# Kernel tuning notes

Measured on AMD Instinct MI355X. Metric: run time of the kernel, lower is better.

## Reference

```python
import jax, jax.numpy as jnp
import numpy as np

N, D_MODEL, D_PE, H = 4096, 512, 16, 8


def setup_inputs() -> dict:
    key = jax.random.key(0)
    ks = jax.random.split(key, 6)
    s = 1.0 / np.sqrt(D_MODEL)
    return {
        "x": jax.random.normal(ks[0], (N, D_MODEL), dtype=jnp.float32),
        "pe": jax.random.normal(ks[1], (N, D_PE), dtype=jnp.float32),
        "w_qkv": jax.random.normal(ks[2], (D_MODEL, 3 * D_MODEL), dtype=jnp.float32) * s,
        "b_qkv": jnp.zeros((3 * D_MODEL,), dtype=jnp.float32),
        "w_pe": jax.random.normal(ks[3], (D_PE, H), dtype=jnp.float32) * (1.0 / np.sqrt(D_PE)),
        "b_pe": jnp.zeros((H,), dtype=jnp.float32),
        "w_out": jax.random.normal(ks[4], (D_MODEL, D_MODEL), dtype=jnp.float32) * s,
        "b_out": jnp.zeros((D_MODEL,), dtype=jnp.float32),
    }


def reference(x, pe, w_qkv, b_qkv, w_pe, b_pe, w_out, b_out):
    n, d = x.shape
    h = w_pe.shape[1]
    hd = d // h
    scale = hd ** -0.5

    qkv = (x @ w_qkv + b_qkv).reshape(n, 3, h, hd)  # [N,3,H,hd]
    q = jnp.transpose(qkv[:, 0], (1, 0, 2))  # [H,N,hd]
    k = jnp.transpose(qkv[:, 1], (1, 0, 2))
    v = jnp.transpose(qkv[:, 2], (1, 0, 2))

    pe_proj = pe @ w_pe + b_pe  # [N,H]
    # bias[h,i,j] = pe_proj[j,h] - pe_proj[i,h]  (matches torch unsqueeze/permute)
    pt = pe_proj.T  # [H,N]
    bias = pt[:, None, :] - pt[:, :, None]  # [H,N,N]

    scores = jnp.einsum('hnd,hmd->hnm', q, k) * scale + bias  # [H,N,N]
    attn = jax.nn.softmax(scores, axis=-1)
    out = jnp.einsum('hnm,hmd->hnd', attn, v)  # [H,N,hd]
    out = jnp.transpose(out, (1, 0, 2)).reshape(n, d)
    return out @ w_out + b_out
```

## Files before the change

kernel.cpp:

```cpp
#include <hip/hip_runtime.h>
#include <stdint.h>
#include <stddef.h>


typedef unsigned short u16;
typedef __attribute__((ext_vector_type(8))) short short8;
typedef __attribute__((ext_vector_type(8))) unsigned short us8;
typedef __attribute__((ext_vector_type(4))) unsigned short us4;
typedef __attribute__((ext_vector_type(4))) float floatx4;

__device__ __forceinline__ u16 f2b(float f) {
  union { float f; uint32_t u; } v; v.f = f;
  uint32_t u = v.u;
  return (u16)((u + 0x7fffu + ((u >> 16) & 1u)) >> 16);
}

__device__ __forceinline__ uint32_t pkbf16(float a, float b) {
  union { float f; uint32_t u; } x, y; x.f = a; y.f = b;
  return __builtin_amdgcn_perm(y.u + 0x8000u, x.u + 0x8000u, 0x07060302u);
}

#if __has_builtin(__builtin_amdgcn_exp2f)
__device__ __forceinline__ float fexp2(float x) { return __builtin_amdgcn_exp2f(x); }
#else
__device__ __forceinline__ float fexp2(float x) { return exp2f(x); }
#endif

__device__ __forceinline__ void gld16(const u16* g, u16* l) {
  __builtin_amdgcn_global_load_lds(
      (const __attribute__((address_space(1))) uint32_t*)(const void*)g,
      (__attribute__((address_space(3))) uint32_t*)(void*)l, 16, 0, 0);
}


__device__ __forceinline__ void tr_tile(const float* __restrict__ in,
                                        u16* __restrict__ out, int R, int C,
                                        int bx, int by, u16 (*tile)[33]) {
  int tx = threadIdx.x & 31, ty = threadIdx.x >> 5;
  int c0 = bx * 32, r0 = by * 32;
#pragma unroll
  for (int i = 0; i < 32; i += 8)
    tile[ty + i][tx] = f2b(in[(size_t)(r0 + ty + i) * C + c0 + tx]);
  __syncthreads();
#pragma unroll
  for (int i = 0; i < 32; i += 8)
    out[(size_t)(c0 + ty + i) * R + r0 + tx] = tile[tx][ty + i];
}

__global__ __launch_bounds__(256) void k_prep(
    const float* __restrict__ x, u16* __restrict__ xb,
    const float* __restrict__ w_qkv, u16* __restrict__ wqkvT,
    const float* __restrict__ w_out, u16* __restrict__ woutT,
    const float* __restrict__ pe, const float* __restrict__ w_pe,
    const float* __restrict__ b_pe, float* __restrict__ wexp,
    u16* __restrict__ wpb) {
  __shared__ u16 tile[32][33];
  int b = blockIdx.x;
  if (b < 2048) {
    int i = b * 256 + threadIdx.x;
    float4 v = ((const float4*)x)[i];
    uint2 o = make_uint2(pkbf16(v.x, v.y), pkbf16(v.z, v.w));
    ((uint2*)xb)[i] = o;
  } else if (b < 2816) {
    int idx = b - 2048;
    tr_tile(w_qkv, wqkvT, 512, 1536, idx % 48, idx / 48, tile);
  } else if (b < 3072) {
    int idx = b - 2816;
    tr_tile(w_out, woutT, 512, 512, idx % 16, idx / 16, tile);
  } else {
    int idx = (b - 3072) * 256 + threadIdx.x;
    int h = idx >> 12, n = idx & 4095;
    float acc = b_pe[h];
#pragma unroll
    for (int d = 0; d < 16; ++d) acc = fmaf(pe[n * 16 + d], w_pe[d * 8 + h], acc);
    float w = exp2f(acc * 1.4426950408889634f - 16.0f);
    u16 wb = f2b(w);
    union { uint32_t u; float f; } cv; cv.u = ((uint32_t)wb) << 16;
    wexp[h * 4096 + n] = cv.f;
    int pn = (n & ~31) | (((n >> 2) & 3) << 3) | (((n >> 4) & 1) << 2) | (n & 3);
    wpb[h * 4096 + pn] = wb;
  }
}


__global__ __launch_bounds__(512, 6) void k_gemm_qkv(const u16* __restrict__ A,
                                                     const u16* __restrict__ Bt,
                                                     const float* __restrict__ bias,
                                                     const float* __restrict__ wexp,
                                                     u16* __restrict__ qk,
                                                     u16* __restrict__ vtp) {
  __shared__ __align__(16) u16 smem[24576];
  const int tid = threadIdx.x;
  const int lane = tid & 63, wave = tid >> 6;
  const int colx = lane & 15, quad = lane >> 4;
  const int m0 = blockIdx.y * 64, n0 = blockIdx.x * 128;
  const int wm = wave >> 2, wn = wave & 3;
  const int sc = (lane & 7) ^ ((lane >> 3) & 7);
  const floatx4 fz = {0.f, 0.f, 0.f, 0.f};
  floatx4 acc[2][2];
#pragma unroll
  for (int i = 0; i < 2; ++i)
#pragma unroll
    for (int j = 0; j < 2; ++j) acc[i][j] = fz;

#define PREF_QKV(k0, b)                                                       \
  {                                                                           \
    int rowa = wave * 8 + (lane >> 3);                                        \
    gld16(&A[(size_t)(m0 + rowa) * 512 + (k0) + sc * 8],                      \
          &smem[(b) * 4096 + wave * 512 + lane * 8]);                         \
    _Pragma("unroll") for (int c = 0; c < 2; ++c) {                           \
      int rowb = wave * 16 + c * 8 + (lane >> 3);                             \
      gld16(&Bt[(size_t)(n0 + rowb) * 512 + (k0) + sc * 8],                   \
            &smem[8192 + (b) * 8192 + wave * 1024 + c * 512 + lane * 8]);     \
    }                                                                         \
  }

  PREF_QKV(0, 0);
  __syncthreads();
  for (int it = 0; it < 8; ++it) {
    int cur = it & 1;
    if (it < 7) PREF_QKV((it + 1) * 64, cur ^ 1);
    const u16* As = &smem[cur * 4096];
    const u16* Bs = &smem[8192 + cur * 8192];
#pragma unroll
    for (int kk = 0; kk < 2; ++kk) {
      short8 af[2], bf[2];
#pragma unroll
      for (int i = 0; i < 2; ++i) {
        int row = wm * 32 + i * 16 + colx;
        af[i] = *(const short8*)&As[row * 64 + (((kk * 4 + quad) ^ (colx & 7))) * 8];
      }
#pragma unroll
      for (int j = 0; j < 2; ++j) {
        int row = wn * 32 + j * 16 + colx;
        bf[j] = *(const short8*)&Bs[row * 64 + (((kk * 4 + quad) ^ (colx & 7))) * 8];
      }
#pragma unroll
      for (int i = 0; i < 2; ++i)
#pragma unroll
        for (int j = 0; j < 2; ++j)
          acc[i][j] = __builtin_amdgcn_mfma_f32_16x16x32_bf16(af[i], bf[j], acc[i][j], 0, 0, 0);
    }
    __syncthreads();
  }

  const bool isV = (blockIdx.x >= 8);
  if (!isV) {
#pragma unroll
    for (int j = 0; j < 2; ++j) {
      int c = n0 + wn * 32 + j * 16 + colx;
      float bq = bias[c];
      float qs = (c < 512) ? 0.18033688011112042f : 1.0f;
#pragma unroll
      for (int i = 0; i < 2; ++i)
#pragma unroll
        for (int r = 0; r < 4; ++r) {
          int row = m0 + wm * 32 + i * 16 + quad * 4 + r;
          qk[(size_t)row * 1024 + c] = f2b((acc[i][j][r] + bq) * qs);
        }
    }
  } else {
    const int dv = n0 - 1024;
    u16* Vl = smem;
    const int hh = (dv + wn * 32) >> 6;
#pragma unroll
    for (int j = 0; j < 2; ++j) {
      float bq = bias[n0 + wn * 32 + j * 16 + colx];
#pragma unroll
      for (int i = 0; i < 2; ++i) {
        floatx4 wv = *(const floatx4*)&wexp[hh * 4096 + m0 + wm * 32 + i * 16 + quad * 4];
        us4 o;
#pragma unroll
        for (int r = 0; r < 4; ++r) o[r] = f2b((acc[i][j][r] + bq) * wv[r]);
        int dl = wn * 32 + j * 16 + colx;
        int nc = wm * 32 + quad * 8 + i * 4;
        *(us4*)&Vl[dl * 72 + nc] = o;
      }
    }
    __syncthreads();
#pragma unroll
    for (int t = 0; t < 2; ++t) {
      int idx = t * 512 + tid;
      int dl = idx >> 3, ch = idx & 7;
      *(us8*)&vtp[(size_t)(dv + dl) * 4096 + m0 + ch * 8] =
          *(const us8*)&Vl[dl * 72 + ch * 8];
    }
  }
#undef PREF_QKV
}


__global__ __launch_bounds__(512, 8) void k_flash(const u16* __restrict__ qk,
                                                  const u16* __restrict__ vt,
                                                  const u16* __restrict__ wpb,
                                                  float* __restrict__ opart,
                                                  float* __restrict__ lpart) {
  __shared__ __align__(16) u16 smem[20480];
  float* bufs = (float*)smem;

  const int tid = threadIdx.x;
  const int lane = tid & 63, wave = tid >> 6;
  const int colx = lane & 15, quad = lane >> 4;
  const int ih = wave >> 1, jq = wave & 1;
  const int q0 = blockIdx.x * 64;
  const int h = blockIdx.y;
  const int z = blockIdx.z;
  const int kvb = z * 2048;
  const floatx4 fz = {0.f, 0.f, 0.f, 0.f};

  const int sc = (lane & 7) ^ ((lane >> 3) & 7);
  const int srow = wave * 8 + (lane >> 3);

  {
    int row = tid >> 3, ch = tid & 7;
    *(us8*)&smem[row * 64 + (ch ^ (row & 7)) * 8] =
        *(const us8*)&qk[(size_t)(q0 + row) * 1024 + h * 64 + ch * 8];
  }
  const u16* qptr = qk + (size_t)(kvb + srow) * 1024 + 512 + h * 64 + sc * 8;
  const u16* vptr = vt + (size_t)(h * 64 + srow) * 4096 + kvb + sc * 8;
  const u16* wptr = wpb + h * 4096 + kvb + jq * 32 + quad * 8;
  gld16(qptr, &smem[4096 + wave * 512 + lane * 8]);
  gld16(vptr, &smem[12288 + wave * 512 + lane * 8]);
  qptr += 65536;
  vptr += 64;
  __syncthreads();

  short8 qf[2];
#pragma unroll
  for (int kk = 0; kk < 2; ++kk) {
    int row = ih * 16 + colx;
    qf[kk] = *(const short8*)&smem[row * 64 + (((kk * 4 + quad) ^ (colx & 7))) * 8];
  }

  floatx4 oacc[4], lacc = fz;
#pragma unroll
  for (int cb = 0; cb < 4; ++cb) oacc[cb] = fz;

#define FBODY(CUR, PREF)                                                      \
  {                                                                           \
    short8 wf = *(const short8*)wptr;                                         \
    wptr += 64;                                                               \
    if (PREF) {                                                               \
      gld16(qptr, &smem[4096 + (1 - (CUR)) * 4096 + wave * 512 + lane * 8]);  \
      gld16(vptr, &smem[12288 + (1 - (CUR)) * 4096 + wave * 512 + lane * 8]); \
      qptr += 65536;                                                          \
      vptr += 64;                                                             \
    }                                                                         \
    const u16* Ks = &smem[4096 + (CUR) * 4096];                               \
    const u16* Vts = &smem[12288 + (CUR) * 4096];                             \
    floatx4 sacc[2] = {fz, fz};                                               \
    _Pragma("unroll") for (int j2 = 0; j2 < 2; ++j2) {                        \
      _Pragma("unroll") for (int kk = 0; kk < 2; ++kk) {                      \
        int row = jq * 32 + j2 * 16 + colx;                                   \
        short8 kf = *(const short8*)&Ks[row * 64 +                            \
                                        (((kk * 4 + quad) ^ (colx & 7))) * 8];\
        sacc[j2] =                                                            \
            __builtin_amdgcn_mfma_f32_16x16x32_bf16(kf, qf[kk], sacc[j2], 0, 0, 0); \
      }                                                                       \
    }                                                                         \
    union { uint32_t w[4]; short8 s; } pk;                                    \
    _Pragma("unroll") for (int j2 = 0; j2 < 2; ++j2) {                        \
      float p0 = fexp2(sacc[j2][0]);                                          \
      float p1 = fexp2(sacc[j2][1]);                                          \
      float p2 = fexp2(sacc[j2][2]);                                          \
      float p3 = fexp2(sacc[j2][3]);                                          \
      pk.w[j2 * 2 + 0] = pkbf16(p0, p1);                                      \
      pk.w[j2 * 2 + 1] = pkbf16(p2, p3);                                      \
    }                                                                         \
    _Pragma("unroll") for (int cb = 0; cb < 4; ++cb) {                        \
      int row = cb * 16 + colx;                                               \
      short8 vf = *(const short8*)&Vts[row * 64 +                             \
                                       (((jq * 4 + quad) ^ (colx & 7))) * 8]; \
      oacc[cb] =                                                              \
          __builtin_amdgcn_mfma_f32_16x16x32_bf16(pk.s, vf, oacc[cb], 0, 0, 0); \
    }                                                                         \
    lacc = __builtin_amdgcn_mfma_f32_16x16x32_bf16(pk.s, wf, lacc, 0, 0, 0);  \
    __syncthreads();                                                          \
  }

  for (int t = 0; t < 15; ++t) {
    FBODY(0, 1)
    FBODY(1, 1)
  }
  FBODY(0, 1)
  FBODY(1, 0)
#undef FBODY

  float* b = bufs + ih * 1040;
  if (jq == 1) {
#pragma unroll
    for (int cb = 0; cb < 4; ++cb)
#pragma unroll
      for (int r = 0; r < 4; ++r)
        b[(quad * 4 + r) * 65 + cb * 16 + colx] = oacc[cb][r];
    if (colx == 0)
#pragma unroll
      for (int r = 0; r < 4; ++r) b[(quad * 4 + r) * 65 + 64] = lacc[r];
  }
  __syncthreads();
  if (jq == 0) {
#pragma unroll
    for (int cb = 0; cb < 4; ++cb)
#pragma unroll
      for (int r = 0; r < 4; ++r)
        oacc[cb][r] += b[(quad * 4 + r) * 65 + cb * 16 + colx];
#pragma unroll
    for (int r = 0; r < 4; ++r) lacc[r] += b[(quad * 4 + r) * 65 + 64];
    float* op = opart + (size_t)z * 2097152;
#pragma unroll
    for (int cb = 0; cb < 4; ++cb)
#pragma unroll
      for (int r = 0; r < 4; ++r)
        op[(size_t)(q0 + ih * 16 + quad * 4 + r) * 512 + h * 64 + cb * 16 + colx] =
            oacc[cb][r];
    if (colx == 0)
#pragma unroll
      for (int r = 0; r < 4; ++r)
        lpart[z * 32768 + h * 4096 + q0 + ih * 16 + quad * 4 + r] = lacc[r];
  }
}


__global__ __launch_bounds__(256) void k_comb(const float* __restrict__ opart,
                                              const float* __restrict__ lpart,
                                              u16* __restrict__ ao) {
  int idx = blockIdx.x * 256 + threadIdx.x;
  int n = idx >> 7, d4 = idx & 127;
  int h = d4 >> 4;
  float l = lpart[h * 4096 + n] + lpart[32768 + h * 4096 + n];
  float inv = 1.0f / l;
  float4 o0 = *(const float4*)&opart[(size_t)n * 512 + d4 * 4];
  float4 o1 = *(const float4*)&opart[2097152 + (size_t)n * 512 + d4 * 4];
  us4 o;
  o[0] = f2b((o0.x + o1.x) * inv);
  o[1] = f2b((o0.y + o1.y) * inv);
  o[2] = f2b((o0.z + o1.z) * inv);
  o[3] = f2b((o0.w + o1.w) * inv);
  *(us4*)&ao[(size_t)n * 512 + d4 * 4] = o;
}


__global__ __launch_bounds__(512, 4) void k_gemm_out(const u16* __restrict__ A,
                                                     const u16* __restrict__ Bt,
                                                     const float* __restrict__ bias,
                                                     float* __restrict__ Cout) {
  __shared__ __align__(16) u16 smem[16384];
  const int tid = threadIdx.x;
  const int lane = tid & 63, wave = tid >> 6;
  const int colx = lane & 15, quad = lane >> 4;
  const int m0 = blockIdx.y * 64, n0 = blockIdx.x * 64;
  const int wm = wave >> 2, wn = wave & 3;
  const int sc = (lane & 7) ^ ((lane >> 3) & 7);
  const floatx4 fz = {0.f, 0.f, 0.f, 0.f};
  floatx4 acc[2];
  acc[0] = fz; acc[1] = fz;

#define PREF_OUT(k0, b)                                                       \
  {                                                                           \
    int rowa = wave * 8 + (lane >> 3);                                        \
    gld16(&A[(size_t)(m0 + rowa) * 512 + (k0) + sc * 8],                      \
          &smem[(b) * 4096 + wave * 512 + lane * 8]);                         \
    gld16(&Bt[(size_t)(n0 + rowa) * 512 + (k0) + sc * 8],                     \
          &smem[8192 + (b) * 4096 + wave * 512 + lane * 8]);                  \
  }

  PREF_OUT(0, 0);
  __syncthreads();
  for (int it = 0; it < 8; ++it) {
    int cur = it & 1;
    if (it < 7) PREF_OUT((it + 1) * 64, cur ^ 1);
    const u16* As = &smem[cur * 4096];
    const u16* Bs = &smem[8192 + cur * 4096];
#pragma unroll
    for (int kk = 0; kk < 2; ++kk) {
      short8 af[2], bf;
#pragma unroll
      for (int i = 0; i < 2; ++i) {
        int row = wm * 32 + i * 16 + colx;
        af[i] = *(const short8*)&As[row * 64 + (((kk * 4 + quad) ^ (colx & 7))) * 8];
      }
      {
        int row = wn * 16 + colx;
        bf = *(const short8*)&Bs[row * 64 + (((kk * 4 + quad) ^ (colx & 7))) * 8];
      }
#pragma unroll
      for (int i = 0; i < 2; ++i)
        acc[i] = __builtin_amdgcn_mfma_f32_16x16x32_bf16(af[i], bf, acc[i], 0, 0, 0);
    }
    __syncthreads();
  }
  int c = n0 + wn * 16 + colx;
  float bq = bias[c];
#pragma unroll
  for (int i = 0; i < 2; ++i)
#pragma unroll
    for (int r = 0; r < 4; ++r) {
      int row = m0 + wm * 32 + i * 16 + quad * 4 + r;
      Cout[(size_t)row * 512 + c] = acc[i][r] + bq;
    }
#undef PREF_OUT
}


extern "C" void kernel_launch(void* const* d_in, const int* in_sizes, int n_in,
                              void* d_out, int out_size, void* d_ws, size_t ws_size,
                              hipStream_t stream) {
  const float* x     = (const float*)d_in[0];
  const float* pe    = (const float*)d_in[1];
  const float* w_qkv = (const float*)d_in[2];
  const float* b_qkv = (const float*)d_in[3];
  const float* w_pe  = (const float*)d_in[4];
  const float* b_pe  = (const float*)d_in[5];
  const float* w_out = (const float*)d_in[6];
  const float* b_out = (const float*)d_in[7];
  float* out = (float*)d_out;

  u16* xb    = (u16*)d_ws;
  u16* wqkvT = xb    + 2097152;
  u16* woutT = wqkvT + 786432;
  u16* qk    = woutT + 262144;
  u16* vt    = qk    + 4194304;
  u16* wpb   = vt    + 2097152;
  u16* ao    = wpb   + 32768;
  float* wexp  = (float*)(ao + 2097152);
  float* opart = wexp + 32768;
  float* lpart = opart + 4194304;

  k_prep<<<3200, 256, 0, stream>>>(x, xb, w_qkv, wqkvT, w_out, woutT,
                                   pe, w_pe, b_pe, wexp, wpb);
  k_gemm_qkv<<<dim3(12, 64), 512, 0, stream>>>(xb, wqkvT, b_qkv, wexp, qk, vt);
  k_flash<<<dim3(64, 8, 2), 512, 0, stream>>>(qk, vt, wpb, opart, lpart);
  k_comb<<<2048, 256, 0, stream>>>(opart, lpart, ao);
  k_gemm_out<<<dim3(8, 64), 512, 0, stream>>>(ao, woutT, b_out, out);
}
```

Baseline: 142.2 us.

## Fuse split-KV combine into flash kernel via atomic last-block reduction

Removes the separate combine kernel. Each flash block atomically increments a per-(query tile, head) counter, and whichever of the two KV-split blocks finishes second reads its partner's partial output and normalizer, combines them, and writes bf16 attention output. Q fragments are now loaded straight from global memory instead of staged through LDS, which shrinks shared memory. This trades a kernel launch and a full pass over the partials for threadfences, an atomic, and a flag-zeroing block in the prep kernel.

```diff
diff --git a/kernel.cpp b/kernel.cpp
--- a/kernel.cpp
+++ b/kernel.cpp
@@ -53,7 +53,7 @@
     const float* __restrict__ w_out, u16* __restrict__ woutT,
     const float* __restrict__ pe, const float* __restrict__ w_pe,
     const float* __restrict__ b_pe, float* __restrict__ wexp,
-    u16* __restrict__ wpb) {
+    u16* __restrict__ wpb, int* __restrict__ flags) {
   __shared__ u16 tile[32][33];
   int b = blockIdx.x;
   if (b < 2048) {
@@ -67,7 +67,7 @@
   } else if (b < 3072) {
     int idx = b - 2816;
     tr_tile(w_out, woutT, 512, 512, idx % 16, idx / 16, tile);
-  } else {
+  } else if (b < 3200) {
     int idx = (b - 3072) * 256 + threadIdx.x;
     int h = idx >> 12, n = idx & 4095;
     float acc = b_pe[h];
@@ -79,6 +79,9 @@
     wexp[h * 4096 + n] = cv.f;
     int pn = (n & ~31) | (((n >> 2) & 3) << 3) | (((n >> 4) & 1) << 2) | (n & 3);
     wpb[h * 4096 + pn] = wb;
+  } else {
+    flags[threadIdx.x] = 0;
+    flags[256 + threadIdx.x] = 0;
   }
 }
 
@@ -194,9 +197,12 @@
                                                   const u16* __restrict__ vt,
                                                   const u16* __restrict__ wpb,
                                                   float* __restrict__ opart,
-                                                  float* __restrict__ lpart) {
-  __shared__ __align__(16) u16 smem[20480];
+                                                  float* __restrict__ lpart,
+                                                  u16* __restrict__ ao,
+                                                  int* __restrict__ flags) {
+  __shared__ __align__(16) u16 smem[16384];
   float* bufs = (float*)smem;
+  int* fl = (int*)&smem[16380];
 
   const int tid = threadIdx.x;
   const int lane = tid & 63, wave = tid >> 6;
@@ -211,26 +217,20 @@
   const int sc = (lane & 7) ^ ((lane >> 3) & 7);
   const int srow = wave * 8 + (lane >> 3);
 
-  {
-    int row = tid >> 3, ch = tid & 7;
-    *(us8*)&smem[row * 64 + (ch ^ (row & 7)) * 8] =
-        *(const us8*)&qk[(size_t)(q0 + row) * 1024 + h * 64 + ch * 8];
-  }
+  short8 qf[2];
+#pragma unroll
+  for (int kk = 0; kk < 2; ++kk)
+    qf[kk] = *(const short8*)&qk[(size_t)(q0 + ih * 16 + colx) * 1024 +
+                                 h * 64 + kk * 32 + quad * 8];
+
   const u16* qptr = qk + (size_t)(kvb + srow) * 1024 + 512 + h * 64 + sc * 8;
   const u16* vptr = vt + (size_t)(h * 64 + srow) * 4096 + kvb + sc * 8;
   const u16* wptr = wpb + h * 4096 + kvb + jq * 32 + quad * 8;
-  gld16(qptr, &smem[4096 + wave * 512 + lane * 8]);
-  gld16(vptr, &smem[12288 + wave * 512 + lane * 8]);
+  gld16(qptr, &smem[wave * 512 + lane * 8]);
+  gld16(vptr, &smem[8192 + wave * 512 + lane * 8]);
   qptr += 65536;
   vptr += 64;
   __syncthreads();
-
-  short8 qf[2];
-#pragma unroll
-  for (int kk = 0; kk < 2; ++kk) {
-    int row = ih * 16 + colx;
-    qf[kk] = *(const short8*)&smem[row * 64 + (((kk * 4 + quad) ^ (colx & 7))) * 8];
-  }
 
   floatx4 oacc[4], lacc = fz;
 #pragma unroll
@@ -241,13 +241,13 @@
     short8 wf = *(const short8*)wptr;                                         \
     wptr += 64;                                                               \
     if (PREF) {                                                               \
-      gld16(qptr, &smem[4096 + (1 - (CUR)) * 4096 + wave * 512 + lane * 8]);  \
-      gld16(vptr, &smem[12288 + (1 - (CUR)) * 4096 + wave * 512 + lane * 8]); \
+      gld16(qptr, &smem[(1 - (CUR)) * 4096 + wave * 512 + lane * 8]);         \
+      gld16(vptr, &smem[8192 + (1 - (CUR)) * 4096 + wave * 512 + lane * 8]);  \
       qptr += 65536;                                                          \
       vptr += 64;                                                             \
     }                                                                         \
-    const u16* Ks = &smem[4096 + (CUR) * 4096];                               \
-    const u16* Vts = &smem[12288 + (CUR) * 4096];                             \
+    const u16* Ks = &smem[(CUR) * 4096];                                      \
+    const u16* Vts = &smem[8192 + (CUR) * 4096];                              \
     floatx4 sacc[2] = {fz, fz};                                               \
     _Pragma("unroll") for (int j2 = 0; j2 < 2; ++j2) {                        \
       _Pragma("unroll") for (int kk = 0; kk < 2; ++kk) {                      \
@@ -318,25 +318,27 @@
       for (int r = 0; r < 4; ++r)
         lpart[z * 32768 + h * 4096 + q0 + ih * 16 + quad * 4 + r] = lacc[r];
   }
-}
-
-
-__global__ __launch_bounds__(256) void k_comb(const float* __restrict__ opart,
-                                              const float* __restrict__ lpart,
-                                              u16* __restrict__ ao) {
-  int idx = blockIdx.x * 256 + threadIdx.x;
-  int n = idx >> 7, d4 = idx & 127;
-  int h = d4 >> 4;
-  float l = lpart[h * 4096 + n] + lpart[32768 + h * 4096 + n];
-  float inv = 1.0f / l;
-  float4 o0 = *(const float4*)&opart[(size_t)n * 512 + d4 * 4];
-  float4 o1 = *(const float4*)&opart[2097152 + (size_t)n * 512 + d4 * 4];
-  us4 o;
-  o[0] = f2b((o0.x + o1.x) * inv);
-  o[1] = f2b((o0.y + o1.y) * inv);
-  o[2] = f2b((o0.z + o1.z) * inv);
-  o[3] = f2b((o0.w + o1.w) * inv);
-  *(us4*)&ao[(size_t)n * 512 + d4 * 4] = o;
+  __threadfence();
+  __syncthreads();
+  if (tid == 0) *fl = atomicAdd(&flags[blockIdx.x * 8 + h], 1);
+  __syncthreads();
+  if (*fl == 1 && jq == 0) {
+    __threadfence();
+    const int oz = 1 - z;
+    const float* oo = opart + (size_t)oz * 2097152;
+    const float* ol = lpart + oz * 32768 + h * 4096;
+#pragma unroll
+    for (int r = 0; r < 4; ++r) {
+      int row = q0 + ih * 16 + quad * 4 + r;
+      float inv = 1.0f / (lacc[r] + ol[row]);
+#pragma unroll
+      for (int cb = 0; cb < 4; ++cb) {
+        int col = h * 64 + cb * 16 + colx;
+        ao[(size_t)row * 512 + col] =
+            f2b((oacc[cb][r] + oo[(size_t)row * 512 + col]) * inv);
+      }
+    }
+  }
 }
 
 
@@ -425,11 +427,11 @@
   float* wexp  = (float*)(ao + 2097152);
   float* opart = wexp + 32768;
   float* lpart = opart + 4194304;
-
-  k_prep<<<3200, 256, 0, stream>>>(x, xb, w_qkv, wqkvT, w_out, woutT,
-                                   pe, w_pe, b_pe, wexp, wpb);
+  int* flags   = (int*)(lpart + 65536);
+
+  k_prep<<<3201, 256, 0, stream>>>(x, xb, w_qkv, wqkvT, w_out, woutT,
+                                   pe, w_pe, b_pe, wexp, wpb, flags);
   k_gemm_qkv<<<dim3(12, 64), 512, 0, stream>>>(xb, wqkvT, b_qkv, wexp, qk, vt);
-  k_flash<<<dim3(64, 8, 2), 512, 0, stream>>>(qk, vt, wpb, opart, lpart);
-  k_comb<<<2048, 256, 0, stream>>>(opart, lpart, ao);
+  k_flash<<<dim3(64, 8, 2), 512, 0, stream>>>(qk, vt, wpb, opart, lpart, ao, flags);
   k_gemm_out<<<dim3(8, 64), 512, 0, stream>>>(ao, woutT, b_out, out);
 }
```

After: 403.0 us. +183.5%, slower.
